# Kernel tuning notes

Measured on AMD Instinct MI355X. Metric: run time of the kernel, lower is better.

Reference implementation:

```python
import jax, jax.numpy as jnp
import numpy as np

DIM = 2                 # spatial dimension (fixed to 2 in the source)
T = 6                   # number_of_time_points
DT = 1.0 / (T - 1)


def _mlp(z, W1, b1, W2, b2, W3, b3):
    # Linear_Tanh(4->10), Linear_Tanh(10->10), Linear(10->3)
    h = jnp.tanh(z @ W1 + b1)
    h = jnp.tanh(h @ W2 + b2)
    return h @ W3 + b3


def _sym_block(o):
    # o[...,3] -> symmetric 2x2 block: off-diag o[...,0], diag exp(o[...,1]), exp(o[...,2])
    off = o[..., 0]
    row0 = jnp.stack([jnp.exp(o[..., 1]), off], axis=-1)
    row1 = jnp.stack([off, jnp.exp(o[..., 2])], axis=-1)
    return jnp.stack([row0, row1], axis=-2)


def _kernel_blocks(x, y, params):
    # x: [b, nx, 2], y: [b, ny, 2] -> pairwise 2x2 kernel blocks [b, nx, ny, 2, 2]
    b, nx, _ = x.shape
    ny = y.shape[1]
    xx = jnp.broadcast_to(x[:, :, None, :], (b, nx, ny, DIM))
    yy = jnp.broadcast_to(y[:, None, :, :], (b, nx, ny, DIM))
    K1 = _sym_block(_mlp(jnp.concatenate([xx, yy], axis=-1), *params))
    K2 = _sym_block(_mlp(jnp.concatenate([yy, xx], axis=-1), *params))
    return 0.5 * (K1 + K2)


def _matvec(K, q):
    # block-matrix vector product: K [b,nx,ny,2,2] @ q [b,ny,2] -> [b,nx,2]
    return jnp.einsum('bxyij,byj->bxi', K, q)


def _forward(q_0, template_points, control_points, W1, b1, W2, b2, W3, b3):
    params = (W1, b1, W2, b2, W3, b3)
    bts = q_0.shape[0]
    p = jnp.broadcast_to(control_points[None], (bts,) + control_points.shape)
    p_t, q_t = [p], [q_0]

    def ham(pp, qq):
        dh_dq = _matvec(_kernel_blocks(pp, pp, params), qq)
        return 0.5 * jnp.sum(qq * dh_dq), dh_dq

    # Hamiltonian shooting: T steps of symplectic-Euler-like integration
    for _ in range(T):
        pc, qc = p_t[-1], q_t[-1]
        (_, dh_dq), dh_dp = jax.value_and_grad(ham, has_aux=True)(pc, qc)
        p_t.append(pc + DT * dh_dq)
        q_t.append(qc - DT * dh_dp)

    # flow the template points along the time-varying velocity field
    x = jnp.broadcast_to(template_points[None], (bts,) + template_points.shape)
    for pc, qc in zip(p_t, q_t):
        x = x + DT * _matvec(_kernel_blocks(x, pc, params), qc)
    return x


def setup_inputs() -> dict:
    key = jax.random.key(0)
    ks = jax.random.split(key, 8)
    bts, ncp, ntpl, H = 16, 64, 2048, 10
    # 8x8 control-point grid over [-2.5, 2.5]^2 (compute_grid with margin 0)
    ax = jnp.linspace(-2.5, 2.5, 8, dtype=jnp.float32)
    gx, gy = jnp.meshgrid(ax, ax, indexing='ij')
    control_points = jnp.stack([gx, gy], axis=-1).reshape(ncp, DIM)
    template_points = jax.random.normal(ks[0], (ntpl, DIM), dtype=jnp.float32)
    q_0 = 0.05 * jax.random.normal(ks[1], (bts, ncp, DIM), dtype=jnp.float32)
    W1 = 0.5 * jax.random.normal(ks[2], (2 * DIM, H), dtype=jnp.float32)
    b1 = jnp.zeros((H,), dtype=jnp.float32)
    W2 = 0.5 * jax.random.normal(ks[3], (H, H), dtype=jnp.float32)
    b2 = jnp.zeros((H,), dtype=jnp.float32)
    W3 = 0.5 * jax.random.normal(ks[4], (H, DIM * (DIM + 1) // 2), dtype=jnp.float32)
    b3 = jnp.zeros((DIM * (DIM + 1) // 2,), dtype=jnp.float32)
    return {'q_0': q_0, 'template_points': template_points, 'control_points': control_points,
            'W1': W1, 'b1': b1, 'W2': W2, 'b2': b2, 'W3': W3, 'b3': b3}


def reference(q_0, template_points, control_points, W1, b1, W2, b2, W3, b3):
    return _forward(q_0, template_points, control_points, W1, b1, W2, b2, W3, b3)
```

## Files before the change

kernel.cpp:

```cpp
#include <hip/hip_runtime.h>

#define NCP    64
#define BTS    16
#define NTPL   2048
#define TSTEPS 6
#define DTF    0.2f
#define L2E    1.4426950408889634f

__device__ __forceinline__ float fast_rcp(float x) { return __builtin_amdgcn_rcpf(x); }
__device__ __forceinline__ float fexp2(float x)    { return __builtin_amdgcn_exp2f(x); }
__device__ __forceinline__ float fast_tanh(float x) {
    float e = __expf(2.0f * x);
    return 1.0f - 2.0f * fast_rcp(1.0f + e);
}

__device__ __forceinline__ void kblock(
    float x0, float x1, float p0, float p1,
    const float (&w)[180], const float* __restrict__ wt,
    float& M00, float& M01, float& M11)
{
    float ra[10], rb[10];
#pragma unroll
    for (int k = 0; k < 10; ++k) {
        float ta = fmaf(p1, w[30 + k],
                   fmaf(p0, w[20 + k],
                   fmaf(x1, w[10 + k],
                   fmaf(x0, w[k], w[40 + k]))));
        float tb = fmaf(x1, w[30 + k],
                   fmaf(x0, w[20 + k],
                   fmaf(p1, w[10 + k],
                   fmaf(p0, w[k], w[40 + k]))));
        ra[k] = fast_rcp(1.0f + fexp2(ta));
        rb[k] = fast_rcp(1.0f + fexp2(tb));
    }
    float ua[10], ub[10];
#pragma unroll
    for (int k = 0; k < 10; ++k) {
        float bb = wt[150 + k];
        ua[k] = fmaf(ra[0], w[50 + k], bb);
        ub[k] = fmaf(rb[0], w[50 + k], bb);
    }
#pragma unroll
    for (int c = 1; c < 10; ++c) {
#pragma unroll
        for (int k = 0; k < 10; ++k) {
            float ww = w[50 + c * 10 + k];
            ua[k] = fmaf(ra[c], ww, ua[k]);
            ub[k] = fmaf(rb[c], ww, ub[k]);
        }
    }
    float Oa = wt[190], Ob = wt[190];
    float T1a = wt[191], T1b = wt[191];
    float T2a = wt[192], T2b = wt[192];
#pragma unroll
    for (int c = 0; c < 10; ++c) {
        float r2a = fast_rcp(1.0f + fexp2(ua[c]));
        float r2b = fast_rcp(1.0f + fexp2(ub[c]));
        Oa  = fmaf(r2a, w[150 + c], Oa);   Ob  = fmaf(r2b, w[150 + c], Ob);
        T1a = fmaf(r2a, w[160 + c], T1a);  T1b = fmaf(r2b, w[160 + c], T1b);
        T2a = fmaf(r2a, w[170 + c], T2a);  T2b = fmaf(r2b, w[170 + c], T2b);
    }
    M00 = fexp2(T1a) + fexp2(T1b);
    M01 = Oa + Ob;
    M11 = fexp2(T2a) + fexp2(T2b);
}

__device__ __forceinline__ void kblock4(
    const float (&x0)[4], const float (&x1)[4], float p0, float p1,
    const float (&w)[180], const float* __restrict__ wt,
    float (&M00)[4], float (&M01)[4], float (&M11)[4])
{
    float r[8][10];
#pragma unroll
    for (int k = 0; k < 10; ++k) {
        float w0 = w[k], w1 = w[10 + k], w2 = w[20 + k], w3 = w[30 + k];
        float bb = w[40 + k];
#pragma unroll
        for (int m = 0; m < 4; ++m) {
            float ta = fmaf(p1, w3, fmaf(p0, w2,
                       fmaf(x1[m], w1, fmaf(x0[m], w0, bb))));
            float tb = fmaf(x1[m], w3, fmaf(x0[m], w2,
                       fmaf(p1, w1, fmaf(p0, w0, bb))));
            r[2 * m][k]     = fast_rcp(1.0f + fexp2(ta));
            r[2 * m + 1][k] = fast_rcp(1.0f + fexp2(tb));
        }
    }
    float u[8][10];
#pragma unroll
    for (int k = 0; k < 10; ++k) {
        float bb = wt[150 + k];
        float ww = w[50 + k];
#pragma unroll
        for (int s = 0; s < 8; ++s) u[s][k] = fmaf(r[s][0], ww, bb);
    }
#pragma unroll
    for (int c = 1; c < 10; ++c) {
#pragma unroll
        for (int k = 0; k < 10; ++k) {
            float ww = w[50 + c * 10 + k];
#pragma unroll
            for (int s = 0; s < 8; ++s) u[s][k] = fmaf(r[s][c], ww, u[s][k]);
        }
    }
    float O[8], A[8], B[8];
#pragma unroll
    for (int s = 0; s < 8; ++s) { O[s] = wt[190]; A[s] = wt[191]; B[s] = wt[192]; }
#pragma unroll
    for (int c = 0; c < 10; ++c) {
        float c0 = w[150 + c], c1 = w[160 + c], c2 = w[170 + c];
#pragma unroll
        for (int s = 0; s < 8; ++s) {
            float g = fast_rcp(1.0f + fexp2(u[s][c]));
            O[s] = fmaf(g, c0, O[s]);
            A[s] = fmaf(g, c1, A[s]);
            B[s] = fmaf(g, c2, B[s]);
        }
    }
#pragma unroll
    for (int m = 0; m < 4; ++m) {
        M00[m] = fexp2(A[2 * m]) + fexp2(A[2 * m + 1]);
        M01[m] = O[2 * m] + O[2 * m + 1];
        M11[m] = fexp2(B[2 * m]) + fexp2(B[2 * m + 1]);
    }
}

__device__ __forceinline__ void load_w(const float* __restrict__ wt,
                                       int lane, float (&w)[180])
{
    float c0 = wt[lane];
    float c1 = wt[64 + lane];
    float c2 = wt[128 + lane];
#pragma unroll
    for (int t = 0; t < 180; ++t) {
        int src = (t < 150) ? t : (t + 10);
        int ch = src >> 6, ix = src & 63;
        float v = (ch == 0) ? c0 : (ch == 1) ? c1 : c2;
        w[t] = __shfl(v, ix);
    }
}

__global__ __launch_bounds__(64, 1)
void shoot_step(const float* __restrict__ q0, const float* __restrict__ cp,
                const float* __restrict__ p_in, const float* __restrict__ q_in,
                float* __restrict__ p_out, float* __restrict__ q_out,
                const float* __restrict__ W1, const float* __restrict__ b1,
                const float* __restrict__ W2, const float* __restrict__ b2,
                const float* __restrict__ W3, const float* __restrict__ b3,
                float* __restrict__ wt, int first)
{
    int blk = blockIdx.x;
    if (first && blk == BTS * NCP) {
        int t = threadIdx.x;
        if (t < 40) wt[t] = 2.0f * L2E * W1[t];
        if (t < 10) wt[40 + t] = 2.0f * L2E * b1[t];
        for (int i = t; i < 100; i += 64) wt[50 + i] = -4.0f * L2E * W2[i];
        if (t < 10) {
            float s = b2[t];
            for (int c = 0; c < 10; ++c) s += W2[c * 10 + t];
            wt[150 + t] = 2.0f * L2E * s;
            wt[160 + t] = -W3[t * 3 + 0];
            wt[170 + t] = -2.0f * L2E * W3[t * 3 + 1];
            wt[180 + t] = -2.0f * L2E * W3[t * 3 + 2];
        }
        if (t < 3) {
            float s = b3[t];
            for (int c = 0; c < 10; ++c) s += W3[c * 3 + t];
            wt[190 + t] = (t == 0) ? 0.5f * s : fmaf(L2E, s, -1.0f);
        }
        return;
    }

    int batch = blk >> 6;
    int a = blk & (NCP - 1);
    int b = threadIdx.x;

    float pax, pay, qax, qay, pbx, pby, qbx, qby;
    if (first) {
        pax = cp[2 * a]; pay = cp[2 * a + 1];
        pbx = cp[2 * b]; pby = cp[2 * b + 1];
        qax = q0[(batch * NCP + a) * 2 + 0]; qay = q0[(batch * NCP + a) * 2 + 1];
        qbx = q0[(batch * NCP + b) * 2 + 0]; qby = q0[(batch * NCP + b) * 2 + 1];
    } else {
        const float* pB = p_in + batch * NCP * 2;
        const float* qB = q_in + batch * NCP * 2;
        pax = pB[a * 2 + 0]; pay = pB[a * 2 + 1];
        qax = qB[a * 2 + 0]; qay = qB[a * 2 + 1];
        pbx = pB[b * 2 + 0]; pby = pB[b * 2 + 1];
        qbx = qB[b * 2 + 0]; qby = qB[b * 2 + 1];
    }

    float dhq_x = 0.f, dhq_y = 0.f;
    float g_x = 0.f, g_y = 0.f;
    float cross = fmaf(qax, qby, qay * qbx);

#pragma unroll
    for (int e = 0; e < 2; ++e) {
        float z0 = e ? pbx : pax;
        float z1 = e ? pby : pay;
        float z2 = e ? pax : pbx;
        float z3 = e ? pay : pby;

        float h1[10];
#pragma unroll
        for (int k = 0; k < 10; ++k) {
            float u = fmaf(z3, W1[30 + k],
                      fmaf(z2, W1[20 + k],
                      fmaf(z1, W1[10 + k],
                      fmaf(z0, W1[k], b1[k]))));
            h1[k] = fast_tanh(u);
        }
        float u2[10];
#pragma unroll
        for (int k = 0; k < 10; ++k) u2[k] = b2[k];
#pragma unroll
        for (int c = 0; c < 10; ++c) {
#pragma unroll
            for (int k = 0; k < 10; ++k) u2[k] = fmaf(h1[c], W2[c * 10 + k], u2[k]);
        }
        float h2[10];
        float o0 = b3[0], o1 = b3[1], o2 = b3[2];
#pragma unroll
        for (int c = 0; c < 10; ++c) {
            h2[c] = fast_tanh(u2[c]);
            o0 = fmaf(h2[c], W3[c * 3 + 0], o0);
            o1 = fmaf(h2[c], W3[c * 3 + 1], o1);
            o2 = fmaf(h2[c], W3[c * 3 + 2], o2);
        }
        float e1 = __expf(o1), e2 = __expf(o2);

        dhq_x = fmaf(0.5f, fmaf(e1, qbx, o0 * qby), dhq_x);
        dhq_y = fmaf(0.5f, fmaf(o0, qbx, e2 * qby), dhq_y);

        float d0 = cross;
        float d1 = e1 * qax * qbx;
        float d2 = e2 * qay * qby;

        float du2[10];
#pragma unroll
        for (int c = 0; c < 10; ++c) {
            float dh2 = fmaf(W3[c * 3 + 0], d0,
                        fmaf(W3[c * 3 + 1], d1, W3[c * 3 + 2] * d2));
            du2[c] = dh2 * (1.0f - h2[c] * h2[c]);
        }
        float du1[10];
#pragma unroll
        for (int c = 0; c < 10; ++c) {
            float dh1 = 0.f;
#pragma unroll
            for (int k = 0; k < 10; ++k) dh1 = fmaf(W2[c * 10 + k], du2[k], dh1);
            du1[c] = dh1 * (1.0f - h1[c] * h1[c]);
        }
        int c0 = e ? 2 : 0;
        float ga = 0.f, gb = 0.f;
#pragma unroll
        for (int k = 0; k < 10; ++k) {
            ga = fmaf(W1[(0 + c0) * 10 + k], du1[k], ga);
            gb = fmaf(W1[(1 + c0) * 10 + k], du1[k], gb);
        }
        g_x = fmaf(0.5f, ga, g_x);
        g_y = fmaf(0.5f, gb, g_y);
    }

#pragma unroll
    for (int off = 32; off > 0; off >>= 1) {
        dhq_x += __shfl_xor(dhq_x, off);
        dhq_y += __shfl_xor(dhq_y, off);
        g_x   += __shfl_xor(g_x, off);
        g_y   += __shfl_xor(g_y, off);
    }

    if (b == 0) {
        float* pO = p_out + (batch * NCP + a) * 2;
        float* qO = q_out + (batch * NCP + a) * 2;
        pO[0] = fmaf(DTF, dhq_x, pax);
        pO[1] = fmaf(DTF, dhq_y, pay);
        qO[0] = fmaf(-DTF, g_x, qax);
        qO[1] = fmaf(-DTF, g_y, qay);
    }
}

__global__ __launch_bounds__(256, 1)
void flow_step0(const float* __restrict__ tpl, const float* __restrict__ cp,
                const float* __restrict__ q0, float* __restrict__ out,
                const float* __restrict__ wt)
{
    int i = blockIdx.x * 4 + (threadIdx.x >> 6);
    int j = threadIdx.x & 63;

    float w[180];
    load_w(wt, j, w);

    float x0 = tpl[2 * i], x1 = tpl[2 * i + 1];
    float p0 = cp[2 * j],  p1 = cp[2 * j + 1];

    float M00, M01, M11;
    kblock(x0, x1, p0, p1, w, wt, M00, M01, M11);

    const float2* __restrict__ q = (const float2*)q0;
#pragma unroll
    for (int bt = 0; bt < BTS; ++bt) {
        float2 qq = q[bt * NCP + j];
        float vx = fmaf(M00, qq.x, M01 * qq.y);
        float vy = fmaf(M01, qq.x, M11 * qq.y);
#pragma unroll
        for (int off = 32; off > 0; off >>= 1) {
            vx += __shfl_xor(vx, off);
            vy += __shfl_xor(vy, off);
        }
        if (j == 0) {
            out[((size_t)bt * NTPL + i) * 2 + 0] = fmaf(DTF, vx, x0);
            out[((size_t)bt * NTPL + i) * 2 + 1] = fmaf(DTF, vy, x1);
        }
    }
}

__global__ __launch_bounds__(256, 1)
void flow_rest(const float* __restrict__ p_hist, const float* __restrict__ q_hist,
               float* __restrict__ out, const float* __restrict__ wt)
{
    int wid = blockIdx.x * 4 + (threadIdx.x >> 6);
    int j = threadIdx.x & 63;
    int u0 = wid * 4;
    int batch = u0 >> 11;
    int i0 = u0 & (NTPL - 1);

    float w[180];
    load_w(wt, j, w);

    const float2* __restrict__ ph = (const float2*)p_hist;
    const float2* __restrict__ qh = (const float2*)q_hist;

    size_t ob = ((size_t)batch * NTPL + i0) * 2;
    float x0[4], x1[4];
#pragma unroll
    for (int m = 0; m < 4; ++m) {
        x0[m] = out[ob + 2 * m];
        x1[m] = out[ob + 2 * m + 1];
    }

#pragma unroll
    for (int s = 0; s < TSTEPS; ++s) {
        int idx = ((s + 1) * BTS + batch) * NCP + j;
        float2 P = ph[idx];
        float2 Q = qh[idx];
        float M00[4], M01[4], M11[4];
        kblock4(x0, x1, P.x, P.y, w, wt, M00, M01, M11);
        float vx[4], vy[4];
#pragma unroll
        for (int m = 0; m < 4; ++m) {
            vx[m] = fmaf(M00[m], Q.x, M01[m] * Q.y);
            vy[m] = fmaf(M01[m], Q.x, M11[m] * Q.y);
        }
#pragma unroll
        for (int off = 32; off > 0; off >>= 1) {
#pragma unroll
            for (int m = 0; m < 4; ++m) {
                vx[m] += __shfl_xor(vx[m], off);
                vy[m] += __shfl_xor(vy[m], off);
            }
        }
#pragma unroll
        for (int m = 0; m < 4; ++m) {
            x0[m] = fmaf(DTF, vx[m], x0[m]);
            x1[m] = fmaf(DTF, vy[m], x1[m]);
        }
    }

    if (j == 0) {
#pragma unroll
        for (int m = 0; m < 4; ++m) {
            out[ob + 2 * m]     = x0[m];
            out[ob + 2 * m + 1] = x1[m];
        }
    }
}

extern "C" void kernel_launch(void* const* d_in, const int* in_sizes, int n_in,
                              void* d_out, int out_size, void* d_ws, size_t ws_size,
                              hipStream_t stream)
{
    const float* q0  = (const float*)d_in[0];
    const float* tpl = (const float*)d_in[1];
    const float* cp  = (const float*)d_in[2];
    const float* W1  = (const float*)d_in[3];
    const float* b1  = (const float*)d_in[4];
    const float* W2  = (const float*)d_in[5];
    const float* b2  = (const float*)d_in[6];
    const float* W3  = (const float*)d_in[7];
    const float* b3  = (const float*)d_in[8];
    float* out = (float*)d_out;

    float* ws = (float*)d_ws;
    const int slab = BTS * NCP * 2;
    float* p_hist = ws;
    float* q_hist = ws + (size_t)7 * slab;
    float* wt     = ws + (size_t)14 * slab;

    shoot_step<<<BTS * NCP + 1, 64, 0, stream>>>(
        q0, cp, nullptr, nullptr,
        p_hist + (size_t)1 * slab, q_hist + (size_t)1 * slab,
        W1, b1, W2, b2, W3, b3, wt, 1);
    for (int s = 1; s < TSTEPS; ++s) {
        shoot_step<<<BTS * NCP, 64, 0, stream>>>(
            q0, cp,
            p_hist + (size_t)s * slab, q_hist + (size_t)s * slab,
            p_hist + (size_t)(s + 1) * slab, q_hist + (size_t)(s + 1) * slab,
            W1, b1, W2, b2, W3, b3, wt, 0);
    }

    flow_step0<<<NTPL / 4, 256, 0, stream>>>(tpl, cp, q0, out, wt);
    flow_rest<<<BTS * NTPL / 16, 256, 0, stream>>>(p_hist, q_hist, out, wt);
}
```

Before: 300.2 us.

## Fuse all shooting steps into one persistent per-batch kernel with shared state

```diff
diff --git a/kernel.cpp b/kernel.cpp
--- a/kernel.cpp
+++ b/kernel.cpp
@@ -139,21 +139,19 @@
     }
 }
 
-__global__ __launch_bounds__(64, 1)
-void shoot_step(const float* __restrict__ q0, const float* __restrict__ cp,
-                const float* __restrict__ p_in, const float* __restrict__ q_in,
-                float* __restrict__ p_out, float* __restrict__ q_out,
-                const float* __restrict__ W1, const float* __restrict__ b1,
-                const float* __restrict__ W2, const float* __restrict__ b2,
-                const float* __restrict__ W3, const float* __restrict__ b3,
-                float* __restrict__ wt, int first)
-{
-    int blk = blockIdx.x;
-    if (first && blk == BTS * NCP) {
+__global__ __launch_bounds__(512, 2)
+void shoot_all(const float* __restrict__ q0, const float* __restrict__ cp,
+               const float* __restrict__ W1, const float* __restrict__ b1,
+               const float* __restrict__ W2, const float* __restrict__ b2,
+               const float* __restrict__ W3, const float* __restrict__ b3,
+               float* __restrict__ p_hist, float* __restrict__ q_hist,
+               float* __restrict__ wt)
+{
+    if (blockIdx.x == BTS) {
         int t = threadIdx.x;
         if (t < 40) wt[t] = 2.0f * L2E * W1[t];
         if (t < 10) wt[40 + t] = 2.0f * L2E * b1[t];
-        for (int i = t; i < 100; i += 64) wt[50 + i] = -4.0f * L2E * W2[i];
+        if (t < 100) wt[50 + t] = -4.0f * L2E * W2[t];
         if (t < 10) {
             float s = b2[t];
             for (int c = 0; c < 10; ++c) s += W2[c * 10 + t];
@@ -170,112 +168,129 @@
         return;
     }
 
-    int batch = blk >> 6;
-    int a = blk & (NCP - 1);
-    int b = threadIdx.x;
-
-    float pax, pay, qax, qay, pbx, pby, qbx, qby;
-    if (first) {
-        pax = cp[2 * a]; pay = cp[2 * a + 1];
-        pbx = cp[2 * b]; pby = cp[2 * b + 1];
-        qax = q0[(batch * NCP + a) * 2 + 0]; qay = q0[(batch * NCP + a) * 2 + 1];
-        qbx = q0[(batch * NCP + b) * 2 + 0]; qby = q0[(batch * NCP + b) * 2 + 1];
-    } else {
-        const float* pB = p_in + batch * NCP * 2;
-        const float* qB = q_in + batch * NCP * 2;
-        pax = pB[a * 2 + 0]; pay = pB[a * 2 + 1];
-        qax = qB[a * 2 + 0]; qay = qB[a * 2 + 1];
-        pbx = pB[b * 2 + 0]; pby = pB[b * 2 + 1];
-        qbx = qB[b * 2 + 0]; qby = qB[b * 2 + 1];
-    }
-
-    float dhq_x = 0.f, dhq_y = 0.f;
-    float g_x = 0.f, g_y = 0.f;
-    float cross = fmaf(qax, qby, qay * qbx);
-
-#pragma unroll
-    for (int e = 0; e < 2; ++e) {
-        float z0 = e ? pbx : pax;
-        float z1 = e ? pby : pay;
-        float z2 = e ? pax : pbx;
-        float z3 = e ? pay : pby;
-
-        float h1[10];
-#pragma unroll
-        for (int k = 0; k < 10; ++k) {
-            float u = fmaf(z3, W1[30 + k],
-                      fmaf(z2, W1[20 + k],
-                      fmaf(z1, W1[10 + k],
-                      fmaf(z0, W1[k], b1[k]))));
-            h1[k] = fast_tanh(u);
-        }
-        float u2[10];
-#pragma unroll
-        for (int k = 0; k < 10; ++k) u2[k] = b2[k];
-#pragma unroll
-        for (int c = 0; c < 10; ++c) {
-#pragma unroll
-            for (int k = 0; k < 10; ++k) u2[k] = fmaf(h1[c], W2[c * 10 + k], u2[k]);
-        }
-        float h2[10];
-        float o0 = b3[0], o1 = b3[1], o2 = b3[2];
-#pragma unroll
-        for (int c = 0; c < 10; ++c) {
-            h2[c] = fast_tanh(u2[c]);
-            o0 = fmaf(h2[c], W3[c * 3 + 0], o0);
-            o1 = fmaf(h2[c], W3[c * 3 + 1], o1);
-            o2 = fmaf(h2[c], W3[c * 3 + 2], o2);
-        }
-        float e1 = __expf(o1), e2 = __expf(o2);
-
-        dhq_x = fmaf(0.5f, fmaf(e1, qbx, o0 * qby), dhq_x);
-        dhq_y = fmaf(0.5f, fmaf(o0, qbx, e2 * qby), dhq_y);
-
-        float d0 = cross;
-        float d1 = e1 * qax * qbx;
-        float d2 = e2 * qay * qby;
-
-        float du2[10];
-#pragma unroll
-        for (int c = 0; c < 10; ++c) {
-            float dh2 = fmaf(W3[c * 3 + 0], d0,
-                        fmaf(W3[c * 3 + 1], d1, W3[c * 3 + 2] * d2));
-            du2[c] = dh2 * (1.0f - h2[c] * h2[c]);
-        }
-        float du1[10];
-#pragma unroll
-        for (int c = 0; c < 10; ++c) {
-            float dh1 = 0.f;
-#pragma unroll
-            for (int k = 0; k < 10; ++k) dh1 = fmaf(W2[c * 10 + k], du2[k], dh1);
-            du1[c] = dh1 * (1.0f - h1[c] * h1[c]);
-        }
-        int c0 = e ? 2 : 0;
-        float ga = 0.f, gb = 0.f;
-#pragma unroll
-        for (int k = 0; k < 10; ++k) {
-            ga = fmaf(W1[(0 + c0) * 10 + k], du1[k], ga);
-            gb = fmaf(W1[(1 + c0) * 10 + k], du1[k], gb);
-        }
-        g_x = fmaf(0.5f, ga, g_x);
-        g_y = fmaf(0.5f, gb, g_y);
-    }
-
-#pragma unroll
-    for (int off = 32; off > 0; off >>= 1) {
-        dhq_x += __shfl_xor(dhq_x, off);
-        dhq_y += __shfl_xor(dhq_y, off);
-        g_x   += __shfl_xor(g_x, off);
-        g_y   += __shfl_xor(g_y, off);
-    }
-
-    if (b == 0) {
-        float* pO = p_out + (batch * NCP + a) * 2;
-        float* qO = q_out + (batch * NCP + a) * 2;
-        pO[0] = fmaf(DTF, dhq_x, pax);
-        pO[1] = fmaf(DTF, dhq_y, pay);
-        qO[0] = fmaf(-DTF, g_x, qax);
-        qO[1] = fmaf(-DTF, g_y, qay);
+    int batch = blockIdx.x;
+    int wv = threadIdx.x >> 6;
+    int b  = threadIdx.x & 63;
+
+    __shared__ float P[NCP][2], Q[NCP][2];
+    if (threadIdx.x < NCP) {
+        int t = threadIdx.x;
+        P[t][0] = cp[2 * t];
+        P[t][1] = cp[2 * t + 1];
+        Q[t][0] = q0[(batch * NCP + t) * 2 + 0];
+        Q[t][1] = q0[(batch * NCP + t) * 2 + 1];
+    }
+    __syncthreads();
+
+    for (int s = 0; s < TSTEPS; ++s) {
+        float np[8][2], nq[8][2];
+
+#pragma unroll
+        for (int sub = 0; sub < 8; ++sub) {
+            int a = (sub << 3) | wv;
+            float pax = P[a][0], pay = P[a][1];
+            float qax = Q[a][0], qay = Q[a][1];
+            float pbx = P[b][0], pby = P[b][1];
+            float qbx = Q[b][0], qby = Q[b][1];
+
+            float dhq_x = 0.f, dhq_y = 0.f;
+            float g_x = 0.f, g_y = 0.f;
+            float cross = fmaf(qax, qby, qay * qbx);
+
+#pragma unroll
+            for (int e = 0; e < 2; ++e) {
+                float z0 = e ? pbx : pax;
+                float z1 = e ? pby : pay;
+                float z2 = e ? pax : pbx;
+                float z3 = e ? pay : pby;
+
+                float h1[10];
+#pragma unroll
+                for (int k = 0; k < 10; ++k) {
+                    float u = fmaf(z3, W1[30 + k],
+                              fmaf(z2, W1[20 + k],
+                              fmaf(z1, W1[10 + k],
+                              fmaf(z0, W1[k], b1[k]))));
+                    h1[k] = fast_tanh(u);
+                }
+                float u2[10];
+#pragma unroll
+                for (int k = 0; k < 10; ++k) u2[k] = b2[k];
+#pragma unroll
+                for (int c = 0; c < 10; ++c) {
+#pragma unroll
+                    for (int k = 0; k < 10; ++k) u2[k] = fmaf(h1[c], W2[c * 10 + k], u2[k]);
+                }
+                float h2[10];
+                float o0 = b3[0], o1 = b3[1], o2 = b3[2];
+#pragma unroll
+                for (int c = 0; c < 10; ++c) {
+                    h2[c] = fast_tanh(u2[c]);
+                    o0 = fmaf(h2[c], W3[c * 3 + 0], o0);
+                    o1 = fmaf(h2[c], W3[c * 3 + 1], o1);
+                    o2 = fmaf(h2[c], W3[c * 3 + 2], o2);
+                }
+                float e1 = __expf(o1), e2 = __expf(o2);
+
+                dhq_x = fmaf(0.5f, fmaf(e1, qbx, o0 * qby), dhq_x);
+                dhq_y = fmaf(0.5f, fmaf(o0, qbx, e2 * qby), dhq_y);
+
+                float d0 = cross;
+                float d1 = e1 * qax * qbx;
+                float d2 = e2 * qay * qby;
+
+                float du2[10];
+#pragma unroll
+                for (int c = 0; c < 10; ++c) {
+                    float dh2 = fmaf(W3[c * 3 + 0], d0,
+                                fmaf(W3[c * 3 + 1], d1, W3[c * 3 + 2] * d2));
+                    du2[c] = dh2 * (1.0f - h2[c] * h2[c]);
+                }
+                float du1[10];
+#pragma unroll
+                for (int c = 0; c < 10; ++c) {
+                    float dh1 = 0.f;
+#pragma unroll
+                    for (int k = 0; k < 10; ++k) dh1 = fmaf(W2[c * 10 + k], du2[k], dh1);
+                    du1[c] = dh1 * (1.0f - h1[c] * h1[c]);
+                }
+                int c0 = e ? 2 : 0;
+                float ga = 0.f, gb = 0.f;
+#pragma unroll
+                for (int k = 0; k < 10; ++k) {
+                    ga = fmaf(W1[(0 + c0) * 10 + k], du1[k], ga);
+                    gb = fmaf(W1[(1 + c0) * 10 + k], du1[k], gb);
+                }
+                g_x = fmaf(0.5f, ga, g_x);
+                g_y = fmaf(0.5f, gb, g_y);
+            }
+
+#pragma unroll
+            for (int off = 32; off > 0; off >>= 1) {
+                dhq_x += __shfl_xor(dhq_x, off);
+                dhq_y += __shfl_xor(dhq_y, off);
+                g_x   += __shfl_xor(g_x, off);
+                g_y   += __shfl_xor(g_y, off);
+            }
+            np[sub][0] = fmaf(DTF, dhq_x, pax);
+            np[sub][1] = fmaf(DTF, dhq_y, pay);
+            nq[sub][0] = fmaf(-DTF, g_x, qax);
+            nq[sub][1] = fmaf(-DTF, g_y, qay);
+        }
+
+        __syncthreads();
+        if (b == 0) {
+#pragma unroll
+            for (int sub = 0; sub < 8; ++sub) {
+                int a = (sub << 3) | wv;
+                P[a][0] = np[sub][0]; P[a][1] = np[sub][1];
+                Q[a][0] = nq[sub][0]; Q[a][1] = nq[sub][1];
+                size_t o = (((size_t)(s + 1) * BTS + batch) * NCP + a) * 2;
+                p_hist[o] = np[sub][0]; p_hist[o + 1] = np[sub][1];
+                q_hist[o] = nq[sub][0]; q_hist[o + 1] = nq[sub][1];
+            }
+        }
+        __syncthreads();
     }
 }
 
@@ -396,18 +411,8 @@
     float* q_hist = ws + (size_t)7 * slab;
     float* wt     = ws + (size_t)14 * slab;
 
-    shoot_step<<<BTS * NCP + 1, 64, 0, stream>>>(
-        q0, cp, nullptr, nullptr,
-        p_hist + (size_t)1 * slab, q_hist + (size_t)1 * slab,
-        W1, b1, W2, b2, W3, b3, wt, 1);
-    for (int s = 1; s < TSTEPS; ++s) {
-        shoot_step<<<BTS * NCP, 64, 0, stream>>>(
-            q0, cp,
-            p_hist + (size_t)s * slab, q_hist + (size_t)s * slab,
-            p_hist + (size_t)(s + 1) * slab, q_hist + (size_t)(s + 1) * slab,
-            W1, b1, W2, b2, W3, b3, wt, 0);
-    }
-
+    shoot_all<<<BTS + 1, 512, 0, stream>>>(q0, cp, W1, b1, W2, b2, W3, b3,
+                                           p_hist, q_hist, wt);
     flow_step0<<<NTPL / 4, 256, 0, stream>>>(tpl, cp, q0, out, wt);
     flow_rest<<<BTS * NTPL / 16, 256, 0, stream>>>(p_hist, q_hist, out, wt);
 }
```

Result: slower. 510.7 us (+70.1%).

## Fuse first shooting step with flow step zero and register-cache MLP weights

Applied to the files above, without the earlier changes.

```diff
diff --git a/kernel.cpp b/kernel.cpp
--- a/kernel.cpp
+++ b/kernel.cpp
@@ -14,9 +14,102 @@
     return 1.0f - 2.0f * fast_rcp(1.0f + e);
 }
 
-__device__ __forceinline__ void kblock(
+__device__ __forceinline__ void load_raw_w(
+    const float* __restrict__ W1, const float* __restrict__ b1,
+    const float* __restrict__ W2, const float* __restrict__ W3,
+    int lane, float (&w)[180])
+{
+    float cA = (lane < 40) ? W1[lane] : (lane < 50 ? b1[lane - 40] : 0.f);
+    float cB0 = W2[lane];
+    float cB1 = (lane < 36) ? W2[64 + lane] : 0.f;
+    float cC  = (lane < 30) ? W3[lane] : 0.f;
+#pragma unroll
+    for (int t = 0; t < 50; ++t)  w[t] = __shfl(cA, t);
+#pragma unroll
+    for (int t = 0; t < 64; ++t)  w[50 + t] = __shfl(cB0, t);
+#pragma unroll
+    for (int t = 0; t < 36; ++t)  w[114 + t] = __shfl(cB1, t);
+#pragma unroll
+    for (int t = 0; t < 30; ++t)  w[150 + t] = __shfl(cC, t);
+}
+
+__device__ __forceinline__ void load_w(const float* __restrict__ wt,
+                                       int lane, float (&w)[180])
+{
+    float c0 = wt[lane];
+    float c1 = wt[64 + lane];
+    float c2 = wt[128 + lane];
+#pragma unroll
+    for (int t = 0; t < 180; ++t) {
+        int src = (t < 150) ? t : (t + 10);
+        int ch = src >> 6, ix = src & 63;
+        float v = (ch == 0) ? c0 : (ch == 1) ? c1 : c2;
+        w[t] = __shfl(v, ix);
+    }
+}
+
+__device__ __forceinline__ void kblock4(
+    const float (&x0)[4], const float (&x1)[4], float p0, float p1,
+    const float (&w)[180], const float* __restrict__ wt,
+    float (&M00)[4], float (&M01)[4], float (&M11)[4])
+{
+    float r[8][10];
+#pragma unroll
+    for (int k = 0; k < 10; ++k) {
+        float w0 = w[k], w1 = w[10 + k], w2 = w[20 + k], w3 = w[30 + k];
+        float bb = w[40 + k];
+#pragma unroll
+        for (int m = 0; m < 4; ++m) {
+            float ta = fmaf(p1, w3, fmaf(p0, w2,
+                       fmaf(x1[m], w1, fmaf(x0[m], w0, bb))));
+            float tb = fmaf(x1[m], w3, fmaf(x0[m], w2,
+                       fmaf(p1, w1, fmaf(p0, w0, bb))));
+            r[2 * m][k]     = fast_rcp(1.0f + fexp2(ta));
+            r[2 * m + 1][k] = fast_rcp(1.0f + fexp2(tb));
+        }
+    }
+    float u[8][10];
+#pragma unroll
+    for (int k = 0; k < 10; ++k) {
+        float bb = wt[150 + k];
+        float ww = w[50 + k];
+#pragma unroll
+        for (int s = 0; s < 8; ++s) u[s][k] = fmaf(r[s][0], ww, bb);
+    }
+#pragma unroll
+    for (int c = 1; c < 10; ++c) {
+#pragma unroll
+        for (int k = 0; k < 10; ++k) {
+            float ww = w[50 + c * 10 + k];
+#pragma unroll
+            for (int s = 0; s < 8; ++s) u[s][k] = fmaf(r[s][c], ww, u[s][k]);
+        }
+    }
+    float O[8], A[8], B[8];
+#pragma unroll
+    for (int s = 0; s < 8; ++s) { O[s] = wt[190]; A[s] = wt[191]; B[s] = wt[192]; }
+#pragma unroll
+    for (int c = 0; c < 10; ++c) {
+        float c0 = w[150 + c], c1 = w[160 + c], c2 = w[170 + c];
+#pragma unroll
+        for (int s = 0; s < 8; ++s) {
+            float g = fast_rcp(1.0f + fexp2(u[s][c]));
+            O[s] = fmaf(g, c0, O[s]);
+            A[s] = fmaf(g, c1, A[s]);
+            B[s] = fmaf(g, c2, B[s]);
+        }
+    }
+#pragma unroll
+    for (int m = 0; m < 4; ++m) {
+        M00[m] = fexp2(A[2 * m]) + fexp2(A[2 * m + 1]);
+        M01[m] = O[2 * m] + O[2 * m + 1];
+        M11[m] = fexp2(B[2 * m]) + fexp2(B[2 * m + 1]);
+    }
+}
+
+__device__ __forceinline__ void kblock_s0(
     float x0, float x1, float p0, float p1,
-    const float (&w)[180], const float* __restrict__ wt,
+    const float (&w)[180], const float (&b2t)[10], const float (&b3t)[3],
     float& M00, float& M01, float& M11)
 {
     float ra[10], rb[10];
@@ -36,7 +129,7 @@
     float ua[10], ub[10];
 #pragma unroll
     for (int k = 0; k < 10; ++k) {
-        float bb = wt[150 + k];
+        float bb = b2t[k];
         ua[k] = fmaf(ra[0], w[50 + k], bb);
         ub[k] = fmaf(rb[0], w[50 + k], bb);
     }
@@ -49,9 +142,9 @@
             ub[k] = fmaf(rb[c], ww, ub[k]);
         }
     }
-    float Oa = wt[190], Ob = wt[190];
-    float T1a = wt[191], T1b = wt[191];
-    float T2a = wt[192], T2b = wt[192];
+    float Oa = b3t[0], Ob = b3t[0];
+    float T1a = b3t[1], T1b = b3t[1];
+    float T2a = b3t[2], T2b = b3t[2];
 #pragma unroll
     for (int c = 0; c < 10; ++c) {
         float r2a = fast_rcp(1.0f + fexp2(ua[c]));
@@ -65,92 +158,134 @@
     M11 = fexp2(T2a) + fexp2(T2b);
 }
 
-__device__ __forceinline__ void kblock4(
-    const float (&x0)[4], const float (&x1)[4], float p0, float p1,
-    const float (&w)[180], const float* __restrict__ wt,
-    float (&M00)[4], float (&M01)[4], float (&M11)[4])
-{
-    float r[8][10];
-#pragma unroll
-    for (int k = 0; k < 10; ++k) {
-        float w0 = w[k], w1 = w[10 + k], w2 = w[20 + k], w3 = w[30 + k];
-        float bb = w[40 + k];
-#pragma unroll
-        for (int m = 0; m < 4; ++m) {
-            float ta = fmaf(p1, w3, fmaf(p0, w2,
-                       fmaf(x1[m], w1, fmaf(x0[m], w0, bb))));
-            float tb = fmaf(x1[m], w3, fmaf(x0[m], w2,
-                       fmaf(p1, w1, fmaf(p0, w0, bb))));
-            r[2 * m][k]     = fast_rcp(1.0f + fexp2(ta));
-            r[2 * m + 1][k] = fast_rcp(1.0f + fexp2(tb));
-        }
-    }
-    float u[8][10];
-#pragma unroll
-    for (int k = 0; k < 10; ++k) {
-        float bb = wt[150 + k];
-        float ww = w[50 + k];
-#pragma unroll
-        for (int s = 0; s < 8; ++s) u[s][k] = fmaf(r[s][0], ww, bb);
-    }
-#pragma unroll
-    for (int c = 1; c < 10; ++c) {
-#pragma unroll
-        for (int k = 0; k < 10; ++k) {
-            float ww = w[50 + c * 10 + k];
-#pragma unroll
-            for (int s = 0; s < 8; ++s) u[s][k] = fmaf(r[s][c], ww, u[s][k]);
-        }
-    }
-    float O[8], A[8], B[8];
-#pragma unroll
-    for (int s = 0; s < 8; ++s) { O[s] = wt[190]; A[s] = wt[191]; B[s] = wt[192]; }
-#pragma unroll
-    for (int c = 0; c < 10; ++c) {
-        float c0 = w[150 + c], c1 = w[160 + c], c2 = w[170 + c];
-#pragma unroll
-        for (int s = 0; s < 8; ++s) {
-            float g = fast_rcp(1.0f + fexp2(u[s][c]));
-            O[s] = fmaf(g, c0, O[s]);
-            A[s] = fmaf(g, c1, A[s]);
-            B[s] = fmaf(g, c2, B[s]);
-        }
-    }
-#pragma unroll
-    for (int m = 0; m < 4; ++m) {
-        M00[m] = fexp2(A[2 * m]) + fexp2(A[2 * m + 1]);
-        M01[m] = O[2 * m] + O[2 * m + 1];
-        M11[m] = fexp2(B[2 * m]) + fexp2(B[2 * m + 1]);
-    }
-}
-
-__device__ __forceinline__ void load_w(const float* __restrict__ wt,
-                                       int lane, float (&w)[180])
-{
-    float c0 = wt[lane];
-    float c1 = wt[64 + lane];
-    float c2 = wt[128 + lane];
-#pragma unroll
-    for (int t = 0; t < 180; ++t) {
-        int src = (t < 150) ? t : (t + 10);
-        int ch = src >> 6, ix = src & 63;
-        float v = (ch == 0) ? c0 : (ch == 1) ? c1 : c2;
-        w[t] = __shfl(v, ix);
+__device__ __forceinline__ void shoot_body(
+    int batch, int a, int b,
+    float pax, float pay, float qax, float qay,
+    float pbx, float pby, float qbx, float qby,
+    const float (&w)[180],
+    const float* __restrict__ b2, const float* __restrict__ b3,
+    float* __restrict__ p_out, float* __restrict__ q_out)
+{
+    float dhq_x = 0.f, dhq_y = 0.f;
+    float g_x = 0.f, g_y = 0.f;
+    float cross = fmaf(qax, qby, qay * qbx);
+
+#pragma unroll
+    for (int e = 0; e < 2; ++e) {
+        float z0 = e ? pbx : pax;
+        float z1 = e ? pby : pay;
+        float z2 = e ? pax : pbx;
+        float z3 = e ? pay : pby;
+
+        float h1[10];
+#pragma unroll
+        for (int k = 0; k < 10; ++k) {
+            float u = fmaf(z3, w[30 + k],
+                      fmaf(z2, w[20 + k],
+                      fmaf(z1, w[10 + k],
+                      fmaf(z0, w[k], w[40 + k]))));
+            h1[k] = fast_tanh(u);
+        }
+        float u2[10];
+#pragma unroll
+        for (int k = 0; k < 10; ++k) u2[k] = b2[k];
+#pragma unroll
+        for (int c = 0; c < 10; ++c) {
+#pragma unroll
+            for (int k = 0; k < 10; ++k) u2[k] = fmaf(h1[c], w[50 + c * 10 + k], u2[k]);
+        }
+        float h2[10];
+        float o0 = b3[0], o1 = b3[1], o2 = b3[2];
+#pragma unroll
+        for (int c = 0; c < 10; ++c) {
+            h2[c] = fast_tanh(u2[c]);
+            o0 = fmaf(h2[c], w[150 + c * 3 + 0], o0);
+            o1 = fmaf(h2[c], w[150 + c * 3 + 1], o1);
+            o2 = fmaf(h2[c], w[150 + c * 3 + 2], o2);
+        }
+        float e1 = __expf(o1), e2 = __expf(o2);
+
+        dhq_x = fmaf(0.5f, fmaf(e1, qbx, o0 * qby), dhq_x);
+        dhq_y = fmaf(0.5f, fmaf(o0, qbx, e2 * qby), dhq_y);
+
+        float d0 = cross;
+        float d1 = e1 * qax * qbx;
+        float d2 = e2 * qay * qby;
+
+        float du2[10];
+#pragma unroll
+        for (int c = 0; c < 10; ++c) {
+            float dh2 = fmaf(w[150 + c * 3 + 0], d0,
+                        fmaf(w[150 + c * 3 + 1], d1, w[150 + c * 3 + 2] * d2));
+            du2[c] = dh2 * (1.0f - h2[c] * h2[c]);
+        }
+        float du1[10];
+#pragma unroll
+        for (int c = 0; c < 10; ++c) {
+            float dh1 = 0.f;
+#pragma unroll
+            for (int k = 0; k < 10; ++k) dh1 = fmaf(w[50 + c * 10 + k], du2[k], dh1);
+            du1[c] = dh1 * (1.0f - h1[c] * h1[c]);
+        }
+        int c0 = e ? 2 : 0;
+        float ga = 0.f, gb = 0.f;
+#pragma unroll
+        for (int k = 0; k < 10; ++k) {
+            ga = fmaf(w[(0 + c0) * 10 + k], du1[k], ga);
+            gb = fmaf(w[(1 + c0) * 10 + k], du1[k], gb);
+        }
+        g_x = fmaf(0.5f, ga, g_x);
+        g_y = fmaf(0.5f, gb, g_y);
+    }
+
+#pragma unroll
+    for (int off = 32; off > 0; off >>= 1) {
+        dhq_x += __shfl_xor(dhq_x, off);
+        dhq_y += __shfl_xor(dhq_y, off);
+        g_x   += __shfl_xor(g_x, off);
+        g_y   += __shfl_xor(g_y, off);
+    }
+
+    if (b == 0) {
+        float* pO = p_out + (batch * NCP + a) * 2;
+        float* qO = q_out + (batch * NCP + a) * 2;
+        pO[0] = fmaf(DTF, dhq_x, pax);
+        pO[1] = fmaf(DTF, dhq_y, pay);
+        qO[0] = fmaf(-DTF, g_x, qax);
+        qO[1] = fmaf(-DTF, g_y, qay);
     }
 }
 
 __global__ __launch_bounds__(64, 1)
-void shoot_step(const float* __restrict__ q0, const float* __restrict__ cp,
-                const float* __restrict__ p_in, const float* __restrict__ q_in,
-                float* __restrict__ p_out, float* __restrict__ q_out,
-                const float* __restrict__ W1, const float* __restrict__ b1,
-                const float* __restrict__ W2, const float* __restrict__ b2,
-                const float* __restrict__ W3, const float* __restrict__ b3,
-                float* __restrict__ wt, int first)
+void shoot0_fused(const float* __restrict__ q0, const float* __restrict__ cp,
+                  const float* __restrict__ tpl,
+                  const float* __restrict__ W1, const float* __restrict__ b1,
+                  const float* __restrict__ W2, const float* __restrict__ b2,
+                  const float* __restrict__ W3, const float* __restrict__ b3,
+                  float* __restrict__ p_hist, float* __restrict__ q_hist,
+                  float* __restrict__ wt, float* __restrict__ out)
 {
     int blk = blockIdx.x;
-    if (first && blk == BTS * NCP) {
-        int t = threadIdx.x;
+    int lane = threadIdx.x;
+
+    if (blk < BTS * NCP) {
+        float w[180];
+        load_raw_w(W1, b1, W2, W3, lane, w);
+        int batch = blk >> 6;
+        int a = blk & (NCP - 1);
+        int b = lane;
+        float pax = cp[2 * a], pay = cp[2 * a + 1];
+        float pbx = cp[2 * b], pby = cp[2 * b + 1];
+        float qax = q0[(batch * NCP + a) * 2 + 0], qay = q0[(batch * NCP + a) * 2 + 1];
+        float qbx = q0[(batch * NCP + b) * 2 + 0], qby = q0[(batch * NCP + b) * 2 + 1];
+        shoot_body(batch, a, b, pax, pay, qax, qay, pbx, pby, qbx, qby,
+                   w, b2, b3,
+                   p_hist + (size_t)1 * BTS * NCP * 2,
+                   q_hist + (size_t)1 * BTS * NCP * 2);
+        return;
+    }
+    if (blk == BTS * NCP) {
+        int t = lane;
         if (t < 40) wt[t] = 2.0f * L2E * W1[t];
         if (t < 10) wt[40 + t] = 2.0f * L2E * b1[t];
         for (int i = t; i < 100; i += 64) wt[50 + i] = -4.0f * L2E * W2[i];
@@ -170,131 +305,52 @@
         return;
     }
 
-    int batch = blk >> 6;
-    int a = blk & (NCP - 1);
-    int b = threadIdx.x;
-
-    float pax, pay, qax, qay, pbx, pby, qbx, qby;
-    if (first) {
-        pax = cp[2 * a]; pay = cp[2 * a + 1];
-        pbx = cp[2 * b]; pby = cp[2 * b + 1];
-        qax = q0[(batch * NCP + a) * 2 + 0]; qay = q0[(batch * NCP + a) * 2 + 1];
-        qbx = q0[(batch * NCP + b) * 2 + 0]; qby = q0[(batch * NCP + b) * 2 + 1];
-    } else {
-        const float* pB = p_in + batch * NCP * 2;
-        const float* qB = q_in + batch * NCP * 2;
-        pax = pB[a * 2 + 0]; pay = pB[a * 2 + 1];
-        qax = qB[a * 2 + 0]; qay = qB[a * 2 + 1];
-        pbx = pB[b * 2 + 0]; pby = pB[b * 2 + 1];
-        qbx = qB[b * 2 + 0]; qby = qB[b * 2 + 1];
-    }
-
-    float dhq_x = 0.f, dhq_y = 0.f;
-    float g_x = 0.f, g_y = 0.f;
-    float cross = fmaf(qax, qby, qay * qbx);
-
-#pragma unroll
-    for (int e = 0; e < 2; ++e) {
-        float z0 = e ? pbx : pax;
-        float z1 = e ? pby : pay;
-        float z2 = e ? pax : pbx;
-        float z3 = e ? pay : pby;
-
-        float h1[10];
-#pragma unroll
-        for (int k = 0; k < 10; ++k) {
-            float u = fmaf(z3, W1[30 + k],
-                      fmaf(z2, W1[20 + k],
-                      fmaf(z1, W1[10 + k],
-                      fmaf(z0, W1[k], b1[k]))));
-            h1[k] = fast_tanh(u);
-        }
-        float u2[10];
-#pragma unroll
-        for (int k = 0; k < 10; ++k) u2[k] = b2[k];
-#pragma unroll
-        for (int c = 0; c < 10; ++c) {
-#pragma unroll
-            for (int k = 0; k < 10; ++k) u2[k] = fmaf(h1[c], W2[c * 10 + k], u2[k]);
-        }
-        float h2[10];
-        float o0 = b3[0], o1 = b3[1], o2 = b3[2];
-#pragma unroll
-        for (int c = 0; c < 10; ++c) {
-            h2[c] = fast_tanh(u2[c]);
-            o0 = fmaf(h2[c], W3[c * 3 + 0], o0);
-            o1 = fmaf(h2[c], W3[c * 3 + 1], o1);
-            o2 = fmaf(h2[c], W3[c * 3 + 2], o2);
-        }
-        float e1 = __expf(o1), e2 = __expf(o2);
-
-        dhq_x = fmaf(0.5f, fmaf(e1, qbx, o0 * qby), dhq_x);
-        dhq_y = fmaf(0.5f, fmaf(o0, qbx, e2 * qby), dhq_y);
-
-        float d0 = cross;
-        float d1 = e1 * qax * qbx;
-        float d2 = e2 * qay * qby;
-
-        float du2[10];
-#pragma unroll
-        for (int c = 0; c < 10; ++c) {
-            float dh2 = fmaf(W3[c * 3 + 0], d0,
-                        fmaf(W3[c * 3 + 1], d1, W3[c * 3 + 2] * d2));
-            du2[c] = dh2 * (1.0f - h2[c] * h2[c]);
-        }
-        float du1[10];
-#pragma unroll
-        for (int c = 0; c < 10; ++c) {
-            float dh1 = 0.f;
-#pragma unroll
-            for (int k = 0; k < 10; ++k) dh1 = fmaf(W2[c * 10 + k], du2[k], dh1);
-            du1[c] = dh1 * (1.0f - h1[c] * h1[c]);
-        }
-        int c0 = e ? 2 : 0;
-        float ga = 0.f, gb = 0.f;
-#pragma unroll
-        for (int k = 0; k < 10; ++k) {
-            ga = fmaf(W1[(0 + c0) * 10 + k], du1[k], ga);
-            gb = fmaf(W1[(1 + c0) * 10 + k], du1[k], gb);
-        }
-        g_x = fmaf(0.5f, ga, g_x);
-        g_y = fmaf(0.5f, gb, g_y);
-    }
-
-#pragma unroll
-    for (int off = 32; off > 0; off >>= 1) {
-        dhq_x += __shfl_xor(dhq_x, off);
-        dhq_y += __shfl_xor(dhq_y, off);
-        g_x   += __shfl_xor(g_x, off);
-        g_y   += __shfl_xor(g_y, off);
-    }
-
-    if (b == 0) {
-        float* pO = p_out + (batch * NCP + a) * 2;
-        float* qO = q_out + (batch * NCP + a) * 2;
-        pO[0] = fmaf(DTF, dhq_x, pax);
-        pO[1] = fmaf(DTF, dhq_y, pay);
-        qO[0] = fmaf(-DTF, g_x, qax);
-        qO[1] = fmaf(-DTF, g_y, qay);
-    }
-}
-
-__global__ __launch_bounds__(256, 1)
-void flow_step0(const float* __restrict__ tpl, const float* __restrict__ cp,
-                const float* __restrict__ q0, float* __restrict__ out,
-                const float* __restrict__ wt)
-{
-    int i = blockIdx.x * 4 + (threadIdx.x >> 6);
-    int j = threadIdx.x & 63;
+    int i = blk - (BTS * NCP + 1);
+    int j = lane;
 
     float w[180];
-    load_w(wt, j, w);
+    load_raw_w(W1, b1, W2, W3, j, w);
+
+    float b2t[10], b3t[3];
+#pragma unroll
+    for (int k = 0; k < 10; ++k) {
+        float s = b2[k];
+#pragma unroll
+        for (int c = 0; c < 10; ++c) s += w[50 + c * 10 + k];
+        b2t[k] = 2.0f * L2E * s;
+    }
+#pragma unroll
+    for (int t = 0; t < 3; ++t) {
+        float s = b3[t];
+#pragma unroll
+        for (int c = 0; c < 10; ++c) s += w[150 + c * 3 + t];
+        b3t[t] = (t == 0) ? 0.5f * s : fmaf(L2E, s, -1.0f);
+    }
+#pragma unroll
+    for (int t = 0; t < 50; ++t) w[t] *= 2.0f * L2E;
+#pragma unroll
+    for (int t = 50; t < 150; ++t) w[t] *= -4.0f * L2E;
+    {
+        float c0a[10], c1a[10], c2a[10];
+#pragma unroll
+        for (int k = 0; k < 10; ++k) {
+            c0a[k] = -w[150 + 3 * k];
+            c1a[k] = -2.0f * L2E * w[151 + 3 * k];
+            c2a[k] = -2.0f * L2E * w[152 + 3 * k];
+        }
+#pragma unroll
+        for (int k = 0; k < 10; ++k) {
+            w[150 + k] = c0a[k];
+            w[160 + k] = c1a[k];
+            w[170 + k] = c2a[k];
+        }
+    }
 
     float x0 = tpl[2 * i], x1 = tpl[2 * i + 1];
     float p0 = cp[2 * j],  p1 = cp[2 * j + 1];
 
     float M00, M01, M11;
-    kblock(x0, x1, p0, p1, w, wt, M00, M01, M11);
+    kblock_s0(x0, x1, p0, p1, w, b2t, b3t, M00, M01, M11);
 
     const float2* __restrict__ q = (const float2*)q0;
 #pragma unroll
@@ -312,6 +368,32 @@
             out[((size_t)bt * NTPL + i) * 2 + 1] = fmaf(DTF, vy, x1);
         }
     }
+}
+
+__global__ __launch_bounds__(64, 1)
+void shoot_step(const float* __restrict__ p_in, const float* __restrict__ q_in,
+                float* __restrict__ p_out, float* __restrict__ q_out,
+                const float* __restrict__ W1, const float* __restrict__ b1,
+                const float* __restrict__ W2, const float* __restrict__ b2,
+                const float* __restrict__ W3, const float* __restrict__ b3)
+{
+    int blk = blockIdx.x;
+    int batch = blk >> 6;
+    int a = blk & (NCP - 1);
+    int b = threadIdx.x;
+
+    float w[180];
+    load_raw_w(W1, b1, W2, W3, b, w);
+
+    const float* pB = p_in + batch * NCP * 2;
+    const float* qB = q_in + batch * NCP * 2;
+    float pax = pB[a * 2 + 0], pay = pB[a * 2 + 1];
+    float qax = qB[a * 2 + 0], qay = qB[a * 2 + 1];
+    float pbx = pB[b * 2 + 0], pby = pB[b * 2 + 1];
+    float qbx = qB[b * 2 + 0], qby = qB[b * 2 + 1];
+
+    shoot_body(batch, a, b, pax, pay, qax, qay, pbx, pby, qbx, qby,
+               w, b2, b3, p_out, q_out);
 }
 
 __global__ __launch_bounds__(256, 1)
@@ -396,18 +478,15 @@
     float* q_hist = ws + (size_t)7 * slab;
     float* wt     = ws + (size_t)14 * slab;
 
-    shoot_step<<<BTS * NCP + 1, 64, 0, stream>>>(
-        q0, cp, nullptr, nullptr,
-        p_hist + (size_t)1 * slab, q_hist + (size_t)1 * slab,
-        W1, b1, W2, b2, W3, b3, wt, 1);
+    shoot0_fused<<<BTS * NCP + 1 + NTPL, 64, 0, stream>>>(
+        q0, cp, tpl, W1, b1, W2, b2, W3, b3, p_hist, q_hist, wt, out);
+
     for (int s = 1; s < TSTEPS; ++s) {
         shoot_step<<<BTS * NCP, 64, 0, stream>>>(
-            q0, cp,
             p_hist + (size_t)s * slab, q_hist + (size_t)s * slab,
             p_hist + (size_t)(s + 1) * slab, q_hist + (size_t)(s + 1) * slab,
-            W1, b1, W2, b2, W3, b3, wt, 0);
-    }
-
-    flow_step0<<<NTPL / 4, 256, 0, stream>>>(tpl, cp, q0, out, wt);
+            W1, b1, W2, b2, W3, b3);
+    }
+
     flow_rest<<<BTS * NTPL / 16, 256, 0, stream>>>(p_hist, q_hist, out, wt);
 }
```

After: 299.0 us. Within noise of the previous version (-0.4%).
